# Kernel tuning notes

Hardware: AMD Instinct MI355X
Metric: run time of the kernel (lower is better)

The kernel has to match this reference:

```python
import jax, jax.numpy as jnp
import numpy as np

SIG = [1, 1, 1, 1, -1]  # Cl(4,1)
GA_DIM = 1 << len(SIG)  # 32
IN_F, OUT_F = 128, 128
EPS = 1e-6


def _cayley(sig):
    """Dense Cayley tensor C[a,b,k]: e_a * e_b = C[a,b,a^b] * e_{a^b}.
    Only dim^2 of the dim^3 entries are nonzero (one k per (a,b))."""
    n = len(sig)
    dim = 1 << n
    C = np.zeros((dim, dim, dim), dtype=np.float32)
    for a in range(dim):
        for b in range(dim):
            # reordering sign from moving b's generators past a's
            s = 0
            aa = a >> 1
            while aa:
                s += bin(aa & b).count('1')
                aa >>= 1
            sign = -1.0 if (s & 1) else 1.0
            # metric contribution from repeated generators
            common = a & b
            for i in range(n):
                if common & (1 << i):
                    sign *= sig[i]
            C[a, b, a ^ b] = sign
    return C

_C = jnp.asarray(_cayley(SIG))  # [32,32,32]


def setup_inputs() -> dict:
    key = jax.random.key(0)
    kx, kw = jax.random.split(key)
    x = jax.random.normal(kx, (4096, IN_F, GA_DIM), dtype=jnp.float32)
    std = (2.0 / (IN_F * GA_DIM)) ** 0.5
    w = jax.random.normal(kw, (OUT_F, IN_F, GA_DIM), dtype=jnp.float32) * std
    return {"x": x, "weight": w}


def reference(x, weight):
    # Fold Cayley table into the weight once: Wc[o,f,i,k] = sum_j W[o,f,j] C[i,j,k]
    Wc = jnp.einsum('ofj,ijk->ofik', weight, _C)
    # Geometric linear layer: y[b,o,k] = sum_{f,i} x[b,f,i] Wc[o,f,i,k]
    y = jnp.einsum('bfi,ofik->bok', x, Wc)
    # Manifold normalization: project each output multivector to unit norm
    inv = jax.lax.rsqrt(jnp.sum(y * y, axis=-1, keepdims=True) + EPS)
    return y * inv
```

## Files before the change

### kernel.cpp

```cpp
#include <hip/hip_runtime.h>
#include <stdint.h>

typedef unsigned short ushort_t;
typedef __attribute__((ext_vector_type(8))) __bf16 bf16x8;
typedef __attribute__((ext_vector_type(4))) float  f32x4;


__device__ __forceinline__ unsigned int f2bf(float f) {
    unsigned int u = __float_as_uint(f);
    return (u + 0x7FFFu + ((u >> 16) & 1u)) >> 16;
}

__device__ __forceinline__ float cayley_sign(int a, int b) {
    int s = 0;
    int aa = a >> 1;
    while (aa) { s += __popc(aa & b); aa >>= 1; }
    float sign = (s & 1) ? -1.0f : 1.0f;
    if (a & b & 16) sign = -sign;
    return sign;
}

__device__ __forceinline__ void async16(const ushort_t* g, const ushort_t* l) {
    const __attribute__((address_space(1))) unsigned int* gp =
        (const __attribute__((address_space(1))) unsigned int*)(uintptr_t)g;
    __attribute__((address_space(3))) unsigned int* lp =
        (__attribute__((address_space(3))) unsigned int*)(unsigned int)(uintptr_t)l;
    __builtin_amdgcn_global_load_lds(gp, lp, 16, 0, 0);
}

__global__ __launch_bounds__(256) void prepAB(const float* __restrict__ x,
                                              const float* __restrict__ w,
                                              ushort_t* __restrict__ A_sw,
                                              ushort_t* __restrict__ B_sw) {
    const int k_blk = blockIdx.x;
    const int p_blk = blockIdx.y >> 1;
    const int sub   = blockIdx.y & 1;
    const int t = threadIdx.x;
    const int r  = sub * 64 + (t >> 2);
    const int kq = t & 3;

    const int kt = k_blk >> 1;
    const int kh = k_blk & 1;

    if (blockIdx.z == 0) {
        const int R = p_blk * 128 + r;
        const float* src = x + (size_t)R * 4096 + (size_t)k_blk * 32 + kq * 8;
        float4 a = ((const float4*)src)[0];
        float4 b = ((const float4*)src)[1];
        uint4 pk;
        pk.x = f2bf(a.x) | (f2bf(a.y) << 16);
        pk.y = f2bf(a.z) | (f2bf(a.w) << 16);
        pk.z = f2bf(b.x) | (f2bf(b.y) << 16);
        pk.w = f2bf(b.z) | (f2bf(b.w) << 16);
        const int P = R >> 8, rowp = R & 255;
        *(uint4*)(A_sw + (size_t)(P * 64 + kt) * 16384 + kh * 8192 + kq * 2048 + rowp * 8) = pk;
    } else {
        const int n = p_blk * 128 + r;
        const int o = n >> 5;
        const int kc = n & 31;
        const float* wrow = w + (size_t)o * 4096 + (size_t)k_blk * 32;
        unsigned int pk[4];
#pragma unroll
        for (int pr = 0; pr < 4; ++pr) {
            const int i0 = kq * 8 + pr * 2, i1 = i0 + 1;
            const int j0 = i0 ^ kc, j1 = i1 ^ kc;
            float v0 = wrow[j0] * cayley_sign(i0, j0);
            float v1 = wrow[j1] * cayley_sign(i1, j1);
            pk[pr] = f2bf(v0) | (f2bf(v1) << 16);
        }
        uint4 u = {pk[0], pk[1], pk[2], pk[3]};
        const int P = n >> 8, colp = n & 255;
        *(uint4*)(B_sw + (size_t)(P * 64 + kt) * 16384 + kh * 8192 + kq * 2048 + colp * 8) = u;
    }
}


#define MFMA16(a, b, c) __builtin_amdgcn_mfma_f32_16x16x32_bf16(a, b, c, 0, 0, 0)

#define BLOAD(OFS) do {                                                        \
        bF[0] = *(const bf16x8*)(Bc + bOff + (OFS) + 0 * 128);                 \
        bF[1] = *(const bf16x8*)(Bc + bOff + (OFS) + 1 * 128);                 \
        bF[2] = *(const bf16x8*)(Bc + bOff + (OFS) + 2 * 128);                 \
        bF[3] = *(const bf16x8*)(Bc + bOff + (OFS) + 3 * 128);                 \
    } while (0)

#define GA_PHASE(TMB, KH, PRE_STMT, STAGE_STMT, TAIL_STMT)                     \
    {                                                                          \
        PRE_STMT;                                                              \
        const ushort_t* ap_ = Ac + aOff + (KH) * 8192 + (TMB) * 128;           \
        bf16x8 aF0 = *(const bf16x8*)(ap_ + 0 * 128);                          \
        bf16x8 aF1 = *(const bf16x8*)(ap_ + 1 * 128);                          \
        bf16x8 aF2 = *(const bf16x8*)(ap_ + 2 * 128);                          \
        bf16x8 aF3 = *(const bf16x8*)(ap_ + 3 * 128);                          \
        STAGE_STMT;                                                            \
        __builtin_amdgcn_s_barrier();                                          \
        asm volatile("s_waitcnt lgkmcnt(0)" ::: "memory");                     \
        __builtin_amdgcn_s_setprio(1);                                         \
        acc[(TMB) + 0][0] = MFMA16(aF0, bF[0], acc[(TMB) + 0][0]);             \
        acc[(TMB) + 0][1] = MFMA16(aF0, bF[1], acc[(TMB) + 0][1]);             \
        acc[(TMB) + 0][2] = MFMA16(aF0, bF[2], acc[(TMB) + 0][2]);             \
        acc[(TMB) + 0][3] = MFMA16(aF0, bF[3], acc[(TMB) + 0][3]);             \
        acc[(TMB) + 1][0] = MFMA16(aF1, bF[0], acc[(TMB) + 1][0]);             \
        acc[(TMB) + 1][1] = MFMA16(aF1, bF[1], acc[(TMB) + 1][1]);             \
        acc[(TMB) + 1][2] = MFMA16(aF1, bF[2], acc[(TMB) + 1][2]);             \
        acc[(TMB) + 1][3] = MFMA16(aF1, bF[3], acc[(TMB) + 1][3]);             \
        acc[(TMB) + 2][0] = MFMA16(aF2, bF[0], acc[(TMB) + 2][0]);             \
        acc[(TMB) + 2][1] = MFMA16(aF2, bF[1], acc[(TMB) + 2][1]);             \
        acc[(TMB) + 2][2] = MFMA16(aF2, bF[2], acc[(TMB) + 2][2]);             \
        acc[(TMB) + 2][3] = MFMA16(aF2, bF[3], acc[(TMB) + 2][3]);             \
        acc[(TMB) + 3][0] = MFMA16(aF3, bF[0], acc[(TMB) + 3][0]);             \
        acc[(TMB) + 3][1] = MFMA16(aF3, bF[1], acc[(TMB) + 3][1]);             \
        acc[(TMB) + 3][2] = MFMA16(aF3, bF[2], acc[(TMB) + 3][2]);             \
        acc[(TMB) + 3][3] = MFMA16(aF3, bF[3], acc[(TMB) + 3][3]);             \
        __builtin_amdgcn_s_setprio(0);                                         \
        TAIL_STMT;                                                             \
        __builtin_amdgcn_s_barrier();                                          \
    }

__global__ __launch_bounds__(512, 2) void gemm_norm(const ushort_t* __restrict__ A_sw,
                                                    const ushort_t* __restrict__ B_sw,
                                                    float* __restrict__ out) {
    __shared__ ushort_t As[2][16384];
    __shared__ ushort_t Bs[2][16384];

    int id = blockIdx.x;
    id = (id & 7) * 32 + (id >> 3);
    const int m_blk = id >> 4;
    const int n_blk = id & 15;

    const int t    = threadIdx.x;
    const int wave = t >> 6;
    const int lane = t & 63;
    const int wr = wave >> 2;
    const int wc = wave & 3;
    const int lg = lane >> 4;
    const int lm = lane & 15;

    const int aOff = (lg * 256 + wr * 128 + lm) * 8;
    const int bOff = (lg * 256 + wc * 64  + lm) * 8;

    const ushort_t* aPanel = A_sw + (size_t)m_blk * 64 * 16384;
    const ushort_t* bPanel = B_sw + (size_t)n_blk * 64 * 16384;

    f32x4 acc[8][4];
#pragma unroll
    for (int i = 0; i < 8; ++i)
#pragma unroll
        for (int j = 0; j < 4; ++j)
#pragma unroll
            for (int k = 0; k < 4; ++k) acc[i][j][k] = 0.0f;

    const int so = wave * 1024 + lane * 8;
    const int sl = wave * 1024;

    auto STAGE2 = [&](const ushort_t* src, ushort_t* ldsb) {
        async16(src + so,       ldsb + sl);
        async16(src + so + 512, ldsb + sl + 512);
    };

    const int NT = 64;

    STAGE2(bPanel + 0,             &Bs[0][0]);
    STAGE2(aPanel + 0,             &As[0][0]);
    STAGE2(bPanel + 8192,          &Bs[0][8192]);
    STAGE2(aPanel + 8192,          &As[0][8192]);
    STAGE2(bPanel + 16384,         &Bs[1][0]);
    STAGE2(aPanel + 16384,         &As[1][0]);
    STAGE2(bPanel + 16384 + 8192,  &Bs[1][8192]);
    asm volatile("s_waitcnt vmcnt(10)" ::: "memory");
    __builtin_amdgcn_s_barrier();

#pragma unroll 2
    for (int tt = 0; tt < NT - 2; ++tt) {
        const int b = tt & 1;
        const ushort_t* Ac = &As[b][0];
        const ushort_t* Bc = &Bs[b][0];

        bf16x8 bF[4];

        GA_PHASE(0, 0, BLOAD(0),
                 STAGE2(aPanel + (size_t)(tt + 1) * 16384 + 8192, &As[b ^ 1][8192]),
                 {})
        GA_PHASE(4, 0, {},
                 STAGE2(bPanel + (size_t)(tt + 2) * 16384, &Bs[b][0]),
                 asm volatile("s_waitcnt vmcnt(10)" ::: "memory"))
        GA_PHASE(0, 1, BLOAD(8192),
                 STAGE2(aPanel + (size_t)(tt + 2) * 16384, &As[b][0]),
                 {})
        GA_PHASE(4, 1, {},
                 STAGE2(bPanel + (size_t)(tt + 2) * 16384 + 8192, &Bs[b][8192]),
                 asm volatile("s_waitcnt vmcnt(10)" ::: "memory"))
    }

    {
        const ushort_t* Ac = &As[0][0];
        const ushort_t* Bc = &Bs[0][0];
        bf16x8 bF[4];
        GA_PHASE(0, 0, BLOAD(0),
                 STAGE2(aPanel + (size_t)(NT - 1) * 16384 + 8192, &As[1][8192]),
                 {})
        GA_PHASE(4, 0, {}, {},
                 asm volatile("s_waitcnt vmcnt(8)" ::: "memory"))
        GA_PHASE(0, 1, BLOAD(8192), {}, {})
        GA_PHASE(4, 1, {}, {},
                 asm volatile("s_waitcnt vmcnt(4)" ::: "memory"))
    }
    {
        const ushort_t* Ac = &As[1][0];
        const ushort_t* Bc = &Bs[1][0];
        bf16x8 bF[4];
        GA_PHASE(0, 0, BLOAD(0), {}, {})
        GA_PHASE(4, 0, {}, {},
                 asm volatile("s_waitcnt vmcnt(0)" ::: "memory"))
        GA_PHASE(0, 1, BLOAD(8192), {}, {})
        GA_PHASE(4, 1, {}, {}, {})
    }

    const int row0 = m_blk * 256 + wr * 128;
    const int col0 = n_blk * 256 + wc * 64;
#pragma unroll
    for (int tm = 0; tm < 8; ++tm) {
#pragma unroll
        for (int u = 0; u < 2; ++u) {
#pragma unroll
            for (int reg = 0; reg < 4; ++reg) {
                float v0 = acc[tm][2 * u][reg];
                float v1 = acc[tm][2 * u + 1][reg];
                float p = v0 * v0 + v1 * v1;
                p += __shfl_xor(p, 1);
                p += __shfl_xor(p, 2);
                p += __shfl_xor(p, 4);
                p += __shfl_xor(p, 8);
                const float inv = rsqrtf(p + 1e-6f);
                const int row = row0 + tm * 16 + lg * 4 + reg;
                float* orow = out + (size_t)row * 4096 + col0 + u * 32 + lm;
                orow[0]  = v0 * inv;
                orow[16] = v1 * inv;
            }
        }
    }
}


extern "C" void kernel_launch(void* const* d_in, const int* in_sizes, int n_in,
                              void* d_out, int out_size, void* d_ws, size_t ws_size,
                              hipStream_t stream) {
    const float* x = (const float*)d_in[0];
    const float* w = (const float*)d_in[1];
    float* out = (float*)d_out;

    ushort_t* A_sw = (ushort_t*)d_ws;
    ushort_t* B_sw = A_sw + (size_t)4096 * 4096;

    prepAB<<<dim3(128, 64, 2), 256, 0, stream>>>(x, w, A_sw, B_sw);
    gemm_norm<<<dim3(256), 512, 0, stream>>>(A_sw, B_sw, out);
}
```

Before: 230.4 us.

## Double-buffer LDS fragment reads in registers to overlap with MFMA phases

```diff
diff --git a/kernel.cpp b/kernel.cpp
--- a/kernel.cpp
+++ b/kernel.cpp
@@ -77,43 +77,46 @@
 
 #define MFMA16(a, b, c) __builtin_amdgcn_mfma_f32_16x16x32_bf16(a, b, c, 0, 0, 0)
 
-#define BLOAD(OFS) do {                                                        \
-        bF[0] = *(const bf16x8*)(Bc + bOff + (OFS) + 0 * 128);                 \
-        bF[1] = *(const bf16x8*)(Bc + bOff + (OFS) + 1 * 128);                 \
-        bF[2] = *(const bf16x8*)(Bc + bOff + (OFS) + 2 * 128);                 \
-        bF[3] = *(const bf16x8*)(Bc + bOff + (OFS) + 3 * 128);                 \
+#define RD_A4(d0, d1, d2, d3, base, KH, TMB) do {                              \
+        const ushort_t* _p = (base) + aOff + (KH) * 8192 + (TMB) * 128;        \
+        d0 = *(const bf16x8*)(_p + 0 * 128);                                   \
+        d1 = *(const bf16x8*)(_p + 1 * 128);                                   \
+        d2 = *(const bf16x8*)(_p + 2 * 128);                                   \
+        d3 = *(const bf16x8*)(_p + 3 * 128);                                   \
     } while (0)
 
-#define GA_PHASE(TMB, KH, PRE_STMT, STAGE_STMT, TAIL_STMT)                     \
+#define RD_B4(d0, d1, d2, d3, base, KH) do {                                   \
+        const ushort_t* _p = (base) + bOff + (KH) * 8192;                      \
+        d0 = *(const bf16x8*)(_p + 0 * 128);                                   \
+        d1 = *(const bf16x8*)(_p + 1 * 128);                                   \
+        d2 = *(const bf16x8*)(_p + 2 * 128);                                   \
+        d3 = *(const bf16x8*)(_p + 3 * 128);                                   \
+    } while (0)
+
+#define PHASE(STAGE_STMT, RD_STMT, TMB, A0, A1, A2, A3, TAIL)                  \
     {                                                                          \
-        PRE_STMT;                                                              \
-        const ushort_t* ap_ = Ac + aOff + (KH) * 8192 + (TMB) * 128;           \
-        bf16x8 aF0 = *(const bf16x8*)(ap_ + 0 * 128);                          \
-        bf16x8 aF1 = *(const bf16x8*)(ap_ + 1 * 128);                          \
-        bf16x8 aF2 = *(const bf16x8*)(ap_ + 2 * 128);                          \
-        bf16x8 aF3 = *(const bf16x8*)(ap_ + 3 * 128);                          \
         STAGE_STMT;                                                            \
-        __builtin_amdgcn_s_barrier();                                          \
-        asm volatile("s_waitcnt lgkmcnt(0)" ::: "memory");                     \
+        RD_STMT;                                                               \
+        __builtin_amdgcn_sched_barrier(0);                                     \
         __builtin_amdgcn_s_setprio(1);                                         \
-        acc[(TMB) + 0][0] = MFMA16(aF0, bF[0], acc[(TMB) + 0][0]);             \
-        acc[(TMB) + 0][1] = MFMA16(aF0, bF[1], acc[(TMB) + 0][1]);             \
-        acc[(TMB) + 0][2] = MFMA16(aF0, bF[2], acc[(TMB) + 0][2]);             \
-        acc[(TMB) + 0][3] = MFMA16(aF0, bF[3], acc[(TMB) + 0][3]);             \
-        acc[(TMB) + 1][0] = MFMA16(aF1, bF[0], acc[(TMB) + 1][0]);             \
-        acc[(TMB) + 1][1] = MFMA16(aF1, bF[1], acc[(TMB) + 1][1]);             \
-        acc[(TMB) + 1][2] = MFMA16(aF1, bF[2], acc[(TMB) + 1][2]);             \
-        acc[(TMB) + 1][3] = MFMA16(aF1, bF[3], acc[(TMB) + 1][3]);             \
-        acc[(TMB) + 2][0] = MFMA16(aF2, bF[0], acc[(TMB) + 2][0]);             \
-        acc[(TMB) + 2][1] = MFMA16(aF2, bF[1], acc[(TMB) + 2][1]);             \
-        acc[(TMB) + 2][2] = MFMA16(aF2, bF[2], acc[(TMB) + 2][2]);             \
-        acc[(TMB) + 2][3] = MFMA16(aF2, bF[3], acc[(TMB) + 2][3]);             \
-        acc[(TMB) + 3][0] = MFMA16(aF3, bF[0], acc[(TMB) + 3][0]);             \
-        acc[(TMB) + 3][1] = MFMA16(aF3, bF[1], acc[(TMB) + 3][1]);             \
-        acc[(TMB) + 3][2] = MFMA16(aF3, bF[2], acc[(TMB) + 3][2]);             \
-        acc[(TMB) + 3][3] = MFMA16(aF3, bF[3], acc[(TMB) + 3][3]);             \
+        acc[(TMB) + 0][0] = MFMA16(A0, B0_, acc[(TMB) + 0][0]);                \
+        acc[(TMB) + 0][1] = MFMA16(A0, B1_, acc[(TMB) + 0][1]);                \
+        acc[(TMB) + 0][2] = MFMA16(A0, B2_, acc[(TMB) + 0][2]);                \
+        acc[(TMB) + 0][3] = MFMA16(A0, B3_, acc[(TMB) + 0][3]);                \
+        acc[(TMB) + 1][0] = MFMA16(A1, B0_, acc[(TMB) + 1][0]);                \
+        acc[(TMB) + 1][1] = MFMA16(A1, B1_, acc[(TMB) + 1][1]);                \
+        acc[(TMB) + 1][2] = MFMA16(A1, B2_, acc[(TMB) + 1][2]);                \
+        acc[(TMB) + 1][3] = MFMA16(A1, B3_, acc[(TMB) + 1][3]);                \
+        acc[(TMB) + 2][0] = MFMA16(A2, B0_, acc[(TMB) + 2][0]);                \
+        acc[(TMB) + 2][1] = MFMA16(A2, B1_, acc[(TMB) + 2][1]);                \
+        acc[(TMB) + 2][2] = MFMA16(A2, B2_, acc[(TMB) + 2][2]);                \
+        acc[(TMB) + 2][3] = MFMA16(A2, B3_, acc[(TMB) + 2][3]);                \
+        acc[(TMB) + 3][0] = MFMA16(A3, B0_, acc[(TMB) + 3][0]);                \
+        acc[(TMB) + 3][1] = MFMA16(A3, B1_, acc[(TMB) + 3][1]);                \
+        acc[(TMB) + 3][2] = MFMA16(A3, B2_, acc[(TMB) + 3][2]);                \
+        acc[(TMB) + 3][3] = MFMA16(A3, B3_, acc[(TMB) + 3][3]);                \
         __builtin_amdgcn_s_setprio(0);                                         \
-        TAIL_STMT;                                                             \
+        TAIL;                                                                  \
         __builtin_amdgcn_s_barrier();                                          \
     }
 
@@ -170,50 +173,151 @@
     asm volatile("s_waitcnt vmcnt(10)" ::: "memory");
     __builtin_amdgcn_s_barrier();
 
+    bf16x8 aX0, aX1, aX2, aX3, aY0, aY1, aY2, aY3;
+    bf16x8 bX0, bX1, bX2, bX3, bY0, bY1, bY2, bY3;
+
+    RD_A4(aX0, aX1, aX2, aX3, &As[0][0], 0, 0);
+    RD_B4(bX0, bX1, bX2, bX3, &Bs[0][0], 0);
+
+#define B0_ bX0
+#define B1_ bX1
+#define B2_ bX2
+#define B3_ bX3
+#define C0_ bY0
+#define C1_ bY1
+#define C2_ bY2
+#define C3_ bY3
+
 #pragma unroll 2
     for (int tt = 0; tt < NT - 2; ++tt) {
         const int b = tt & 1;
         const ushort_t* Ac = &As[b][0];
         const ushort_t* Bc = &Bs[b][0];
-
-        bf16x8 bF[4];
-
-        GA_PHASE(0, 0, BLOAD(0),
-                 STAGE2(aPanel + (size_t)(tt + 1) * 16384 + 8192, &As[b ^ 1][8192]),
-                 {})
-        GA_PHASE(4, 0, {},
-                 STAGE2(bPanel + (size_t)(tt + 2) * 16384, &Bs[b][0]),
-                 asm volatile("s_waitcnt vmcnt(10)" ::: "memory"))
-        GA_PHASE(0, 1, BLOAD(8192),
-                 STAGE2(aPanel + (size_t)(tt + 2) * 16384, &As[b][0]),
-                 {})
-        GA_PHASE(4, 1, {},
-                 STAGE2(bPanel + (size_t)(tt + 2) * 16384 + 8192, &Bs[b][8192]),
-                 asm volatile("s_waitcnt vmcnt(10)" ::: "memory"))
+        const ushort_t* An = &As[b ^ 1][0];
+        const ushort_t* Bn = &Bs[b ^ 1][0];
+
+        PHASE(STAGE2(aPanel + (size_t)(tt + 1) * 16384 + 8192, &As[b ^ 1][8192]),
+              RD_A4(aY0, aY1, aY2, aY3, Ac, 0, 4),
+              0, aX0, aX1, aX2, aX3,
+              asm volatile("s_waitcnt vmcnt(8)" ::: "memory"))
+
+        PHASE(STAGE2(bPanel + (size_t)(tt + 2) * 16384, &Bs[b][0]),
+              RD_A4(aX0, aX1, aX2, aX3, Ac, 1, 0); RD_B4(bY0, bY1, bY2, bY3, Bc, 1),
+              4, aY0, aY1, aY2, aY3,
+              {})
+
+#undef B0_
+#undef B1_
+#undef B2_
+#undef B3_
+#define B0_ bY0
+#define B1_ bY1
+#define B2_ bY2
+#define B3_ bY3
+
+        PHASE(STAGE2(aPanel + (size_t)(tt + 2) * 16384, &As[b][0]),
+              RD_A4(aY0, aY1, aY2, aY3, Ac, 1, 4),
+              0, aX0, aX1, aX2, aX3,
+              asm volatile("s_waitcnt vmcnt(8)" ::: "memory"))
+
+        PHASE(STAGE2(bPanel + (size_t)(tt + 2) * 16384 + 8192, &Bs[b][8192]),
+              RD_A4(aX0, aX1, aX2, aX3, An, 0, 0); RD_B4(bX0, bX1, bX2, bX3, Bn, 0),
+              4, aY0, aY1, aY2, aY3,
+              {})
+
+#undef B0_
+#undef B1_
+#undef B2_
+#undef B3_
+#define B0_ bX0
+#define B1_ bX1
+#define B2_ bX2
+#define B3_ bX3
     }
 
     {
         const ushort_t* Ac = &As[0][0];
         const ushort_t* Bc = &Bs[0][0];
-        bf16x8 bF[4];
-        GA_PHASE(0, 0, BLOAD(0),
-                 STAGE2(aPanel + (size_t)(NT - 1) * 16384 + 8192, &As[1][8192]),
-                 {})
-        GA_PHASE(4, 0, {}, {},
-                 asm volatile("s_waitcnt vmcnt(8)" ::: "memory"))
-        GA_PHASE(0, 1, BLOAD(8192), {}, {})
-        GA_PHASE(4, 1, {}, {},
-                 asm volatile("s_waitcnt vmcnt(4)" ::: "memory"))
+        const ushort_t* An = &As[1][0];
+        const ushort_t* Bn = &Bs[1][0];
+
+        PHASE(STAGE2(aPanel + (size_t)(NT - 1) * 16384 + 8192, &As[1][8192]),
+              RD_A4(aY0, aY1, aY2, aY3, Ac, 0, 4),
+              0, aX0, aX1, aX2, aX3,
+              asm volatile("s_waitcnt vmcnt(8)" ::: "memory"))
+        PHASE({},
+              RD_A4(aX0, aX1, aX2, aX3, Ac, 1, 0); RD_B4(bY0, bY1, bY2, bY3, Bc, 1),
+              4, aY0, aY1, aY2, aY3,
+              {})
+#undef B0_
+#undef B1_
+#undef B2_
+#undef B3_
+#define B0_ bY0
+#define B1_ bY1
+#define B2_ bY2
+#define B3_ bY3
+        PHASE({},
+              RD_A4(aY0, aY1, aY2, aY3, Ac, 1, 4),
+              0, aX0, aX1, aX2, aX3,
+              asm volatile("s_waitcnt vmcnt(4)" ::: "memory"))
+        PHASE({},
+              RD_A4(aX0, aX1, aX2, aX3, An, 0, 0); RD_B4(bX0, bX1, bX2, bX3, Bn, 0),
+              4, aY0, aY1, aY2, aY3,
+              {})
+#undef B0_
+#undef B1_
+#undef B2_
+#undef B3_
+#define B0_ bX0
+#define B1_ bX1
+#define B2_ bX2
+#define B3_ bX3
     }
     {
         const ushort_t* Ac = &As[1][0];
         const ushort_t* Bc = &Bs[1][0];
-        bf16x8 bF[4];
-        GA_PHASE(0, 0, BLOAD(0), {}, {})
-        GA_PHASE(4, 0, {}, {},
-                 asm volatile("s_waitcnt vmcnt(0)" ::: "memory"))
-        GA_PHASE(0, 1, BLOAD(8192), {}, {})
-        GA_PHASE(4, 1, {}, {}, {})
+
+        PHASE({},
+              RD_A4(aY0, aY1, aY2, aY3, Ac, 0, 4),
+              0, aX0, aX1, aX2, aX3,
+              asm volatile("s_waitcnt vmcnt(0)" ::: "memory"))
+        PHASE({},
+              RD_A4(aX0, aX1, aX2, aX3, Ac, 1, 0); RD_B4(bY0, bY1, bY2, bY3, Bc, 1),
+              4, aY0, aY1, aY2, aY3,
+              {})
+#undef B0_
+#undef B1_
+#undef B2_
+#undef B3_
+#define B0_ bY0
+#define B1_ bY1
+#define B2_ bY2
+#define B3_ bY3
+        PHASE({},
+              RD_A4(aY0, aY1, aY2, aY3, Ac, 1, 4),
+              0, aX0, aX1, aX2, aX3,
+              {})
+        {
+            __builtin_amdgcn_s_setprio(1);
+            acc[4][0] = MFMA16(aY0, B0_, acc[4][0]);
+            acc[4][1] = MFMA16(aY0, B1_, acc[4][1]);
+            acc[4][2] = MFMA16(aY0, B2_, acc[4][2]);
+            acc[4][3] = MFMA16(aY0, B3_, acc[4][3]);
+            acc[5][0] = MFMA16(aY1, B0_, acc[5][0]);
+            acc[5][1] = MFMA16(aY1, B1_, acc[5][1]);
+            acc[5][2] = MFMA16(aY1, B2_, acc[5][2]);
+            acc[5][3] = MFMA16(aY1, B3_, acc[5][3]);
+            acc[6][0] = MFMA16(aY2, B0_, acc[6][0]);
+            acc[6][1] = MFMA16(aY2, B1_, acc[6][1]);
+            acc[6][2] = MFMA16(aY2, B2_, acc[6][2]);
+            acc[6][3] = MFMA16(aY2, B3_, acc[6][3]);
+            acc[7][0] = MFMA16(aY3, B0_, acc[7][0]);
+            acc[7][1] = MFMA16(aY3, B1_, acc[7][1]);
+            acc[7][2] = MFMA16(aY3, B2_, acc[7][2]);
+            acc[7][3] = MFMA16(aY3, B3_, acc[7][3]);
+            __builtin_amdgcn_s_setprio(0);
+        }
     }
 
     const int row0 = m_blk * 256 + wr * 128;
```

Result: no change. 229.4 us (-0.5%).
